# Optimization experiments

Measured on AMD Instinct MI355X. Metric: run time of the kernel, lower is better.

Reference implementation:

```python
import jax, jax.numpy as jnp
import numpy as np

EMB_DIM = 600
NN_UNITS = 300
K_FM = 5
B, L = 8, 2048


def fm(x, w0, w, V):
    # x: [B,L,F], w0: [1], w: [F], V: [k,F] -> [B,L,1]
    lin = w0 + x @ w[:, None]                      # [B,L,1]
    p1 = jnp.square(x @ V.T)                       # [B,L,k]
    p2 = jnp.square(x) @ jnp.square(V).T           # [B,L,k]
    inter = 0.5 * jnp.sum(p1 - p2, axis=-1, keepdims=True)
    return lin + inter


def setup_inputs() -> dict:
    key = jax.random.key(0)
    ks = jax.random.split(key, 12)
    s = 0.02
    inp = {
        "stack_input": jax.random.normal(ks[0], (2, B, L, EMB_DIM), jnp.float32),
        "W1": jax.random.normal(ks[1], (EMB_DIM, NN_UNITS), jnp.float32) * s,
        "b1": jnp.zeros((NN_UNITS,), jnp.float32),
        "W2": jax.random.normal(ks[2], (EMB_DIM, NN_UNITS), jnp.float32) * s,
        "b2": jnp.zeros((NN_UNITS,), jnp.float32),
        # FM params for the two concat branches (F = 2*EMB_DIM)
        "fm_cat_w0": jax.random.normal(ks[3], (2, 1), jnp.float32) * s,
        "fm_cat_w": jax.random.normal(ks[4], (2, 2 * EMB_DIM), jnp.float32) * s,
        "fm_cat_V": jax.random.normal(ks[5], (2, K_FM, 2 * EMB_DIM), jnp.float32) * s,
        # FM params for diff(passage,query) and mul(passage,query): order [p_diff, q_diff, p_mul, q_mul]
        "fm_dm_w0": jax.random.normal(ks[6], (4, 1), jnp.float32) * s,
        "fm_dm_w": jax.random.normal(ks[7], (4, EMB_DIM), jnp.float32) * s,
        "fm_dm_V": jax.random.normal(ks[8], (4, K_FM, EMB_DIM), jnp.float32) * s,
    }
    return inp


def reference(stack_input, W1, b1, W2, b2, fm_cat_w0, fm_cat_w, fm_cat_V,
              fm_dm_w0, fm_dm_w, fm_dm_V):
    passage = stack_input[0]   # [B,L,D]
    query = stack_input[1]     # [B,L,D]

    p_dense = jax.nn.relu(passage @ W1 + b1)   # [B,L,U]
    q_dense = jax.nn.relu(query @ W2 + b2)     # [B,L,U]

    scale = 1.0 / np.sqrt(EMB_DIM).astype(np.float32)
    affinity = scale * jnp.einsum('bpu,bqu->bpq', p_dense, q_dense)  # [B,Lp,Lq]

    aligned_p = jax.nn.softmax(affinity, axis=-1)                    # [B,Lp,Lq]
    aligned_q = jax.nn.softmax(jnp.swapaxes(affinity, 1, 2), axis=-1)  # [B,Lq,Lp]

    passage_aligned = jnp.einsum('bpq,bqd->bpd', aligned_p, passage)  # [B,Lp,D]
    query_aligned = jnp.einsum('bqp,bpd->bqd', aligned_q, query)      # [B,Lq,D]

    passage_concat = jnp.concatenate([query_aligned, passage], axis=2)
    query_concat = jnp.concatenate([passage_aligned, query], axis=2)
    passage_diff = query_aligned - passage
    query_diff = passage_aligned - query
    passage_mul = query_aligned * passage
    query_mul = passage_aligned * query

    c1 = fm(passage_concat, fm_cat_w0[0], fm_cat_w[0], fm_cat_V[0])
    c2 = fm(query_concat, fm_cat_w0[1], fm_cat_w[1], fm_cat_V[1])
    c3 = fm(passage_diff, fm_dm_w0[0], fm_dm_w[0], fm_dm_V[0])
    c4 = fm(query_diff, fm_dm_w0[1], fm_dm_w[1], fm_dm_V[1])
    c5 = fm(passage_mul, fm_dm_w0[2], fm_dm_w[2], fm_dm_V[2])
    c6 = fm(query_mul, fm_dm_w0[3], fm_dm_w[3], fm_dm_V[3])

    features_passage = jnp.concatenate([c1, c3, c5], axis=2)  # [B,L,3]
    features_query = jnp.concatenate([c2, c4, c6], axis=2)    # [B,L,3]
    return features_passage, features_query
```

## Files before the change

### kernel.cpp

```cpp
#include <hip/hip_runtime.h>
#include <hip/hip_bf16.h>

#define BATCH 8
#define LEN   2048
#define DIM   600
#define UNITS 300
#define BL    16384

typedef __attribute__((ext_vector_type(4))) float f32x4;
typedef __attribute__((ext_vector_type(8))) short s16x8;

#define PDB_OFF   0ULL
#define WT_OFF    20971520ULL
#define VT_OFF    21954560ULL
#define EXP_OFF   63897600ULL
#define EXPT_OFF  131006464ULL
#define PAB_OFF   198115328ULL
#define QAB_OFF   218038272ULL
#define RS_OFF    237961216ULL
#define CS_OFF    238026752ULL
#define WS_NEED   238092288ULL

#define AF_SCALE 0.040824829046386304f

__device__ __forceinline__ float wave_sum(float v) {
#pragma unroll
  for (int off = 32; off > 0; off >>= 1) v += __shfl_xor(v, off);
  return v;
}

__device__ __forceinline__ ushort f2bf(float f) {
  union { float f; uint u; } x; x.f = f;
  uint r = x.u + 0x7fffu + ((x.u >> 16) & 1u);
  return (ushort)(r >> 16);
}

__device__ __forceinline__ void ldbf8(const ushort* p, float* f) {
  uint4 q = *(const uint4*)p;
  f[0] = __uint_as_float(q.x << 16); f[1] = __uint_as_float(q.x & 0xffff0000u);
  f[2] = __uint_as_float(q.y << 16); f[3] = __uint_as_float(q.y & 0xffff0000u);
  f[4] = __uint_as_float(q.z << 16); f[5] = __uint_as_float(q.z & 0xffff0000u);
  f[6] = __uint_as_float(q.w << 16); f[7] = __uint_as_float(q.w & 0xffff0000u);
}
__device__ __forceinline__ void ldf8(const float* p, float* f) {
  float4 a = *(const float4*)p, b = *(const float4*)(p + 4);
  f[0]=a.x; f[1]=a.y; f[2]=a.z; f[3]=a.w; f[4]=b.x; f[5]=b.y; f[6]=b.z; f[7]=b.w;
}

__device__ __forceinline__ s16x8 pack8(float4 a, float4 b) {
  s16x8 r;
  r[0]=(short)f2bf(a.x); r[1]=(short)f2bf(a.y); r[2]=(short)f2bf(a.z); r[3]=(short)f2bf(a.w);
  r[4]=(short)f2bf(b.x); r[5]=(short)f2bf(b.y); r[6]=(short)f2bf(b.z); r[7]=(short)f2bf(b.w);
  return r;
}

__global__ __launch_bounds__(256) void prep_wt(const float* __restrict__ W1,
                                               const float* __restrict__ W2,
                                               char* __restrict__ wsb) {
  int id = blockIdx.x * 256 + threadIdx.x;
  if (id >= 2 * 384 * 80) return;
  int dir = id / (384 * 80); int rem = id % (384 * 80);
  int n = rem / 80, ko = rem % 80;
  const float* W = dir ? W2 : W1;
  s16x8 v;
#pragma unroll
  for (int e = 0; e < 8; e++) {
    int k = ko * 8 + e;
    float f = (n < 300 && k < 600) ? W[(size_t)k * 300 + n] : 0.f;
    v[e] = (short)f2bf(f);
  }
  ushort* wt = (ushort*)(wsb + WT_OFF) + (size_t)dir * 384 * 640 + (size_t)n * 640 + ko * 8;
  *(s16x8*)wt = v;
}

__global__ __launch_bounds__(256) void prep_vt(const float* __restrict__ stack,
                                               char* __restrict__ wsb) {
  int z = blockIdx.z;
  const float* src = stack + (size_t)z * LEN * DIM;
  ushort* dst = (ushort*)(wsb + VT_OFF) + (size_t)z * 640 * 2048;
  int p0 = blockIdx.x * 64, d0 = blockIdx.y * 64;
  __shared__ float tile[64][65];
  int t = threadIdx.x;
#pragma unroll
  for (int u = 0; u < 16; u++) {
    int id = u * 256 + t; int r = id >> 6, c = id & 63;
    tile[r][c] = (d0 + c < DIM) ? src[(size_t)(p0 + r) * DIM + d0 + c] : 0.f;
  }
  __syncthreads();
#pragma unroll
  for (int u = 0; u < 16; u++) {
    int id = u * 256 + t; int d = id >> 6, c = id & 63;
    dst[(size_t)(d0 + d) * 2048 + p0 + c] = f2bf(tile[c][d]);
  }
}

__global__ __launch_bounds__(256) void transp_bf16(char* __restrict__ wsb) {
  int b = blockIdx.z;
  const ushort* src = (const ushort*)(wsb + EXP_OFF) + (size_t)b * 2048 * 2048;
  ushort* dst = (ushort*)(wsb + EXPT_OFF) + (size_t)b * 2048 * 2048;
  int p0 = blockIdx.y * 64, q0 = blockIdx.x * 64;
  __shared__ ushort tile[64][72];
  int t = threadIdx.x;
#pragma unroll
  for (int u = 0; u < 2; u++) {
    int id = u * 256 + t; int r = id >> 3, c = id & 7;
    *(s16x8*)&tile[r][c * 8] = *(const s16x8*)(src + (size_t)(p0 + r) * 2048 + q0 + c * 8);
  }
  __syncthreads();
#pragma unroll
  for (int u = 0; u < 2; u++) {
    int id = u * 256 + t; int q = id >> 3, c = id & 7;
    s16x8 v;
#pragma unroll
    for (int e = 0; e < 8; e++) v[e] = (short)tile[c * 8 + e][q];
    *(s16x8*)(dst + (size_t)(q0 + q) * 2048 + p0 + c * 8) = v;
  }
}

template<int MODE>
__global__ __launch_bounds__(256) void gemm_nt(const float* __restrict__ stack,
                                               const float* __restrict__ b1,
                                               const float* __restrict__ b2,
                                               char* __restrict__ wsb) {
  constexpr int KS = (MODE == 0) ? 10 : ((MODE == 1) ? 5 : 32);
  const int t = threadIdx.x;
  const int g = (t >> 4) & 3, l16 = t & 15;
  const int wv = t >> 6, wr = wv >> 1, wc = wv & 1;
  __shared__ __align__(16) char smem[34816];
  char* Ab = smem;
  char* Bb = smem + 16384;

  const int z = blockIdx.z;
  const int m0 = blockIdx.y * 128, n0 = blockIdx.x * 128;

  const float* Agf = nullptr;
  const ushort* Agb = nullptr;
  const ushort* Bgb = nullptr;
  int lda = 0, ldb = 0;
  int dir = 0, bat = 0;
  if constexpr (MODE == 0) {
    Agf = stack + (size_t)z * BL * DIM; lda = DIM;
    Bgb = (const ushort*)(wsb + WT_OFF) + (size_t)z * 384 * 640; ldb = 640;
  } else if constexpr (MODE == 1) {
    Agb = (const ushort*)(wsb + PDB_OFF) + (size_t)z * 2048 * 320; lda = 320;
    Bgb = (const ushort*)(wsb + PDB_OFF) + (size_t)16384 * 320 + (size_t)z * 2048 * 320; ldb = 320;
  } else {
    dir = z & 1; bat = z >> 1;
    Agb = (const ushort*)(wsb + (dir ? EXPT_OFF : EXP_OFF)) + (size_t)bat * 2048 * 2048; lda = 2048;
    Bgb = (const ushort*)(wsb + VT_OFF) + ((size_t)dir * 8 + bat) * 640 * 2048; ldb = 2048;
  }

  f32x4 acc[4][4];
#pragma unroll
  for (int i = 0; i < 4; i++)
#pragma unroll
    for (int j = 0; j < 4; j++) { f32x4 zz = {0.f, 0.f, 0.f, 0.f}; acc[i][j] = zz; }

  for (int kt = 0; kt < KS; kt++) {
    int k0 = kt * 64;
#pragma unroll
    for (int u = 0; u < 4; u++) {
      int c = u * 256 + t; int row = c >> 3; int sl = c & 7; int gs = sl ^ (row & 7);
      s16x8 va;
      if constexpr (MODE == 0) {
        int kb = k0 + gs * 8;
        if (kb < DIM) {
          const float* s = Agf + (size_t)(m0 + row) * DIM + kb;
          va = pack8(*(const float4*)s, *(const float4*)(s + 4));
        } else {
          s16x8 zz = {0,0,0,0,0,0,0,0}; va = zz;
        }
      } else {
        va = *(const s16x8*)(Agb + (size_t)(m0 + row) * lda + k0 + gs * 8);
      }
      *(s16x8*)(Ab + row * 128 + sl * 16) = va;
      *(s16x8*)(Bb + row * 128 + sl * 16) =
          *(const s16x8*)(Bgb + (size_t)(n0 + row) * ldb + k0 + gs * 8);
    }
    __syncthreads();
#pragma unroll
    for (int ks = 0; ks < 2; ks++) {
      s16x8 af[4], bf[4];
#pragma unroll
      for (int f = 0; f < 4; f++) {
        int ar = wr * 64 + f * 16 + l16;
        af[f] = *(const s16x8*)(Ab + ar * 128 + (((ks * 4 + g) ^ (ar & 7)) * 16));
        int br = wc * 64 + f * 16 + l16;
        bf[f] = *(const s16x8*)(Bb + br * 128 + (((ks * 4 + g) ^ (br & 7)) * 16));
      }
#pragma unroll
      for (int i = 0; i < 4; i++)
#pragma unroll
        for (int j = 0; j < 4; j++)
          acc[i][j] = __builtin_amdgcn_mfma_f32_16x16x32_bf16(af[i], bf[j], acc[i][j], 0, 0, 0);
    }
    __syncthreads();
  }

  char* eb = smem;
  const float* bias = nullptr;
  const float* sums = nullptr;
  float* rowsum = nullptr; float* colsum = nullptr;
  if constexpr (MODE == 0) bias = z ? b2 : b1;
  if constexpr (MODE == 1) {
    rowsum = (float*)(wsb + RS_OFF) + (size_t)z * 2048;
    colsum = (float*)(wsb + CS_OFF) + (size_t)z * 2048;
  }
  if constexpr (MODE == 2)
    sums = (const float*)(wsb + (dir ? CS_OFF : RS_OFF)) + (size_t)bat * 2048;

  float colpart[4] = {0.f, 0.f, 0.f, 0.f};
#pragma unroll
  for (int fm = 0; fm < 4; fm++) {
#pragma unroll
    for (int i = 0; i < 4; i++) {
      int m = wr * 64 + fm * 16 + 4 * g + i;
      float inv = 1.f;
      if constexpr (MODE == 2) inv = 1.f / sums[m0 + m];
      float rowpart = 0.f;
#pragma unroll
      for (int fn = 0; fn < 4; fn++) {
        int n = wc * 64 + fn * 16 + l16;
        float v = acc[fm][fn][i];
        if constexpr (MODE == 0) {
          int gn = n0 + n;
          v = (gn < UNITS) ? fmaxf(v + bias[gn], 0.f) : 0.f;
        } else if constexpr (MODE == 1) {
          v = __expf(v * AF_SCALE);
          rowpart += v; colpart[fn] += v;
        } else {
          v *= inv;
        }
        *(ushort*)(eb + m * 272 + 2 * n) = f2bf(v);
      }
      if constexpr (MODE == 1) {
        rowpart += __shfl_xor(rowpart, 1);
        rowpart += __shfl_xor(rowpart, 2);
        rowpart += __shfl_xor(rowpart, 4);
        rowpart += __shfl_xor(rowpart, 8);
        if (l16 == 0) atomicAdd(&rowsum[m0 + m], rowpart);
      }
    }
  }
  if constexpr (MODE == 1) {
#pragma unroll
    for (int fn = 0; fn < 4; fn++) {
      float cp = colpart[fn];
      cp += __shfl_xor(cp, 16);
      cp += __shfl_xor(cp, 32);
      if (((t >> 4) & 3) == 0)
        atomicAdd(&colsum[n0 + wc * 64 + fn * 16 + l16], cp);
    }
  }
  __syncthreads();

#pragma unroll
  for (int u = 0; u < 8; u++) {
    int id = u * 256 + t; int m = id >> 4; int c = id & 15;
    s16x8 v = *(const s16x8*)(eb + m * 272 + c * 16);
    int gn = n0 + c * 8;
    if constexpr (MODE == 0) {
      if (gn < 320) {
        ushort* outp = (ushort*)(wsb + PDB_OFF) + (size_t)z * 16384 * 320;
        *(s16x8*)(outp + (size_t)(m0 + m) * 320 + gn) = v;
      }
    } else if constexpr (MODE == 1) {
      ushort* outp = (ushort*)(wsb + EXP_OFF) + (size_t)z * 2048 * 2048;
      *(s16x8*)(outp + (size_t)(m0 + m) * 2048 + gn) = v;
    } else {
      if (gn < 608) {
        ushort* outp = (ushort*)(wsb + (dir ? QAB_OFF : PAB_OFF)) + (size_t)bat * 2048 * 608;
        *(s16x8*)(outp + (size_t)(m0 + m) * 608 + gn) = v;
      }
    }
  }
}

__global__ __launch_bounds__(256) void fm_v2(
    const float* __restrict__ stack, const char* __restrict__ wsb,
    const float* __restrict__ cat_w0, const float* __restrict__ cat_w,
    const float* __restrict__ cat_V, const float* __restrict__ dm_w0,
    const float* __restrict__ dm_w, const float* __restrict__ dm_V,
    float* __restrict__ out)
{
  const int lane = threadIdx.x & 63;
  const int gw = blockIdx.x * 4 + (threadIdx.x >> 6);
  const int branch = gw >> 14;
  const int pos = gw & 16383;
  const ushort* x1 = (const ushort*)(wsb + (branch ? PAB_OFF : QAB_OFF)) + (size_t)pos * 608;
  const float* x2 = stack + (size_t)branch * BL * DIM + (size_t)pos * DIM;
  float* o = out + (size_t)branch * (BL * 3) + (size_t)pos * 3;

  {
    const float* w = cat_w + branch * 1200;
    const float* V = cat_V + (size_t)branch * 6000;
    float accW = 0.f, accP[5] = {}, accQ[5] = {};
    for (int oc = lane; oc < 150; oc += 64) {
      float x[8];
      if (oc < 75) ldbf8(x1 + oc * 8, x);
      else         ldf8(x2 + (oc - 75) * 8, x);
      float wv[8]; ldf8(w + oc * 8, wv);
#pragma unroll
      for (int e = 0; e < 8; e++) accW = fmaf(x[e], wv[e], accW);
#pragma unroll
      for (int k = 0; k < 5; k++) {
        float vv[8]; ldf8(V + k * 1200 + oc * 8, vv);
#pragma unroll
        for (int e = 0; e < 8; e++) {
          float xv = x[e] * vv[e];
          accP[k] += xv;
          accQ[k] = fmaf(xv, xv, accQ[k]);
        }
      }
    }
    float r = wave_sum(accW); float inter = 0.f;
#pragma unroll
    for (int k = 0; k < 5; k++) {
      float P = wave_sum(accP[k]), Q = wave_sum(accQ[k]);
      inter += P * P - Q;
    }
    if (lane == 0) o[0] = cat_w0[branch] + r + 0.5f * inter;
  }
#pragma unroll
  for (int which = 0; which < 2; which++) {
    const int idx = which * 2 + branch;
    const float* w = dm_w + idx * 600;
    const float* V = dm_V + (size_t)idx * 3000;
    float accW = 0.f, accP[5] = {}, accQ[5] = {};
    for (int oc = lane; oc < 75; oc += 64) {
      float a[8], b[8], x[8];
      ldbf8(x1 + oc * 8, a);
      ldf8(x2 + oc * 8, b);
#pragma unroll
      for (int e = 0; e < 8; e++) x[e] = which ? a[e] * b[e] : a[e] - b[e];
      float wv[8]; ldf8(w + oc * 8, wv);
#pragma unroll
      for (int e = 0; e < 8; e++) accW = fmaf(x[e], wv[e], accW);
#pragma unroll
      for (int k = 0; k < 5; k++) {
        float vv[8]; ldf8(V + k * 600 + oc * 8, vv);
#pragma unroll
        for (int e = 0; e < 8; e++) {
          float xv = x[e] * vv[e];
          accP[k] += xv;
          accQ[k] = fmaf(xv, xv, accQ[k]);
        }
      }
    }
    float r = wave_sum(accW); float inter = 0.f;
#pragma unroll
    for (int k = 0; k < 5; k++) {
      float P = wave_sum(accP[k]), Q = wave_sum(accQ[k]);
      inter += P * P - Q;
    }
    if (lane == 0) o[1 + which] = dm_w0[idx] + r + 0.5f * inter;
  }
}

#define PD_OFF   0UL
#define QD_OFF   4915200UL
#define PA_OFF   9830400UL
#define QA_OFF   19660800UL
#define A_OFF    29491200UL
#define ROWM_OFF 33685504UL
#define ROWS_OFF 33687552UL
#define COLM_OFF 33689600UL
#define COLS_OFF 33691648UL
#define PCM_OFF  33693696UL
#define PCS_OFF  33726464UL
#define WS_FB    (33759232UL * 4UL)

__global__ __launch_bounds__(256) void dense_kernel(
    const float* __restrict__ stack, const float* __restrict__ W1,
    const float* __restrict__ b1, const float* __restrict__ W2,
    const float* __restrict__ b2, float* __restrict__ ws)
{
  const int dir = blockIdx.z;
  const float* X = stack + (size_t)dir * BL * DIM;
  const float* W = dir ? W2 : W1;
  const float* bias = dir ? b2 : b1;
  float* C = ws + (dir ? QD_OFF : PD_OFF);
  const int m0 = blockIdx.y * 64;
  const int n0 = blockIdx.x * 64;
  __shared__ float As[32][68];
  __shared__ float Bs[32][68];
  const int t = threadIdx.x;
  const int tx = t & 15, ty = t >> 4;
  float acc[4][4] = {};
  for (int k0 = 0; k0 < DIM; k0 += 32) {
#pragma unroll
    for (int i = 0; i < 8; i++) {
      int idx = i * 256 + t;
      int m = idx >> 5, k = idx & 31;
      int kk = k0 + k;
      As[k][m] = (kk < DIM) ? X[(size_t)(m0 + m) * DIM + kk] : 0.f;
    }
#pragma unroll
    for (int i = 0; i < 8; i++) {
      int idx = i * 256 + t;
      int k = idx >> 6, n = idx & 63;
      int kk = k0 + k, nn = n0 + n;
      Bs[k][n] = (kk < DIM && nn < UNITS) ? W[(size_t)kk * UNITS + nn] : 0.f;
    }
    __syncthreads();
#pragma unroll
    for (int k = 0; k < 32; k++) {
      float a[4], bb[4];
#pragma unroll
      for (int i = 0; i < 4; i++) a[i] = As[k][ty * 4 + i];
#pragma unroll
      for (int j = 0; j < 4; j++) bb[j] = Bs[k][tx * 4 + j];
#pragma unroll
      for (int i = 0; i < 4; i++)
#pragma unroll
        for (int j = 0; j < 4; j++)
          acc[i][j] = fmaf(a[i], bb[j], acc[i][j]);
    }
    __syncthreads();
  }
#pragma unroll
  for (int j = 0; j < 4; j++) {
    int nn = n0 + tx * 4 + j;
    if (nn >= UNITS) continue;
    float bv = bias[nn];
#pragma unroll
    for (int i = 0; i < 4; i++) {
      int mm = m0 + ty * 4 + i;
      float v = acc[i][j] + bv;
      C[(size_t)mm * UNITS + nn] = v > 0.f ? v : 0.f;
    }
  }
}

__global__ __launch_bounds__(256) void affinity_kernel(float* __restrict__ ws, int b)
{
  const float* P = ws + PD_OFF + (size_t)b * LEN * UNITS;
  const float* Q = ws + QD_OFF + (size_t)b * LEN * UNITS;
  float* A = ws + A_OFF;
  const int p0 = blockIdx.y * 64;
  const int q0 = blockIdx.x * 64;
  __shared__ float As[32][68], Bs[32][68];
  const int t = threadIdx.x, tx = t & 15, ty = t >> 4;
  float acc[4][4] = {};
  for (int k0 = 0; k0 < UNITS; k0 += 32) {
#pragma unroll
    for (int i = 0; i < 8; i++) {
      int idx = i * 256 + t;
      int m = idx >> 5, k = idx & 31;
      int kk = k0 + k;
      As[k][m] = (kk < UNITS) ? P[(size_t)(p0 + m) * UNITS + kk] : 0.f;
      Bs[k][m] = (kk < UNITS) ? Q[(size_t)(q0 + m) * UNITS + kk] : 0.f;
    }
    __syncthreads();
#pragma unroll
    for (int k = 0; k < 32; k++) {
      float a[4], bb[4];
#pragma unroll
      for (int i = 0; i < 4; i++) a[i] = As[k][ty * 4 + i];
#pragma unroll
      for (int j = 0; j < 4; j++) bb[j] = Bs[k][tx * 4 + j];
#pragma unroll
      for (int i = 0; i < 4; i++)
#pragma unroll
        for (int j = 0; j < 4; j++)
          acc[i][j] = fmaf(a[i], bb[j], acc[i][j]);
    }
    __syncthreads();
  }
#pragma unroll
  for (int i = 0; i < 4; i++)
#pragma unroll
    for (int j = 0; j < 4; j++)
      A[(size_t)(p0 + ty * 4 + i) * LEN + (q0 + tx * 4 + j)] = acc[i][j] * AF_SCALE;
}

__global__ __launch_bounds__(256) void rowstats_kernel(float* __restrict__ ws)
{
  const float* A = ws + A_OFF;
  float* rowM = ws + ROWM_OFF;
  float* rowS = ws + ROWS_OFF;
  const int p = blockIdx.x;
  const int t = threadIdx.x;
  __shared__ float row[2048];
  __shared__ float red[256];
#pragma unroll
  for (int i = 0; i < 8; i++) row[i * 256 + t] = A[(size_t)p * LEN + i * 256 + t];
  __syncthreads();
  float pm = -3.0e38f;
#pragma unroll
  for (int i = 0; i < 8; i++) pm = fmaxf(pm, row[i * 256 + t]);
  red[t] = pm; __syncthreads();
  for (int off = 128; off > 0; off >>= 1) {
    if (t < off) red[t] = fmaxf(red[t], red[t + off]);
    __syncthreads();
  }
  float m = red[0];
  __syncthreads();
  float ps = 0.f;
#pragma unroll
  for (int i = 0; i < 8; i++) ps += __expf(row[i * 256 + t] - m);
  red[t] = ps; __syncthreads();
  for (int off = 128; off > 0; off >>= 1) {
    if (t < off) red[t] += red[t + off];
    __syncthreads();
  }
  if (t == 0) { rowM[p] = m; rowS[p] = 1.f / red[0]; }
}

__global__ __launch_bounds__(256) void colpart_kernel(float* __restrict__ ws)
{
  const float* A = ws + A_OFF;
  float* pcm = ws + PCM_OFF;
  float* pcs = ws + PCS_OFF;
  const int q = blockIdx.x * 256 + threadIdx.x;
  const int chunk = blockIdx.y;
  const int p0 = chunk * 128;
  float m = -3.0e38f, s = 0.f;
  for (int p = p0; p < p0 + 128; p++) {
    float v = A[(size_t)p * LEN + q];
    float nm = fmaxf(m, v);
    s = s * __expf(m - nm) + __expf(v - nm);
    m = nm;
  }
  pcm[chunk * 2048 + q] = m;
  pcs[chunk * 2048 + q] = s;
}

__global__ __launch_bounds__(256) void colcomb_kernel(float* __restrict__ ws)
{
  const float* pcm = ws + PCM_OFF;
  const float* pcs = ws + PCS_OFF;
  float* colM = ws + COLM_OFF;
  float* colS = ws + COLS_OFF;
  const int q = blockIdx.x * 256 + threadIdx.x;
  float m = -3.0e38f;
#pragma unroll
  for (int c = 0; c < 16; c++) m = fmaxf(m, pcm[c * 2048 + q]);
  float s = 0.f;
#pragma unroll
  for (int c = 0; c < 16; c++) s += pcs[c * 2048 + q] * __expf(pcm[c * 2048 + q] - m);
  colM[q] = m;
  colS[q] = 1.f / s;
}

__global__ __launch_bounds__(256) void aligned_kernel(const float* __restrict__ stack,
                                                      float* __restrict__ ws, int b)
{
  const int transA = blockIdx.z;
  const float* A = ws + A_OFF;
  const float* stM = ws + (transA ? COLM_OFF : ROWM_OFF);
  const float* stS = ws + (transA ? COLS_OFF : ROWS_OFF);
  const float* V = stack + (size_t)transA * BL * DIM + (size_t)b * LEN * DIM;
  float* O = ws + (transA ? QA_OFF : PA_OFF) + (size_t)b * LEN * DIM;
  const int m0 = blockIdx.y * 64;
  const int n0 = blockIdx.x * 64;
  __shared__ float As[32][68], Bs[32][68];
  __shared__ float sM[64], sS[64];
  const int t = threadIdx.x, tx = t & 15, ty = t >> 4;
  if (t < 64) { sM[t] = stM[m0 + t]; sS[t] = stS[m0 + t]; }
  __syncthreads();
  float acc[4][4] = {};
  for (int k0 = 0; k0 < LEN; k0 += 32) {
    if (!transA) {
#pragma unroll
      for (int i = 0; i < 8; i++) {
        int idx = i * 256 + t;
        int m = idx >> 5, k = idx & 31;
        float a = A[(size_t)(m0 + m) * LEN + k0 + k];
        As[k][m] = __expf(a - sM[m]) * sS[m];
      }
    } else {
#pragma unroll
      for (int i = 0; i < 8; i++) {
        int idx = i * 256 + t;
        int k = idx >> 6, m = idx & 63;
        float a = A[(size_t)(k0 + k) * LEN + m0 + m];
        As[k][m] = __expf(a - sM[m]) * sS[m];
      }
    }
#pragma unroll
    for (int i = 0; i < 8; i++) {
      int idx = i * 256 + t;
      int k = idx >> 6, n = idx & 63;
      int nn = n0 + n;
      Bs[k][n] = (nn < DIM) ? V[(size_t)(k0 + k) * DIM + nn] : 0.f;
    }
    __syncthreads();
#pragma unroll
    for (int k = 0; k < 32; k++) {
      float a[4], bb[4];
#pragma unroll
      for (int i = 0; i < 4; i++) a[i] = As[k][ty * 4 + i];
#pragma unroll
      for (int j = 0; j < 4; j++) bb[j] = Bs[k][tx * 4 + j];
#pragma unroll
      for (int i = 0; i < 4; i++)
#pragma unroll
        for (int j = 0; j < 4; j++)
          acc[i][j] = fmaf(a[i], bb[j], acc[i][j]);
    }
    __syncthreads();
  }
#pragma unroll
  for (int i = 0; i < 4; i++)
#pragma unroll
    for (int j = 0; j < 4; j++) {
      int nn = n0 + tx * 4 + j;
      if (nn < DIM) O[(size_t)(m0 + ty * 4 + i) * DIM + nn] = acc[i][j];
    }
}

__global__ __launch_bounds__(256) void fm_kernel(
    const float* __restrict__ stack, const float* __restrict__ ws,
    const float* __restrict__ cat_w0, const float* __restrict__ cat_w,
    const float* __restrict__ cat_V, const float* __restrict__ dm_w0,
    const float* __restrict__ dm_w, const float* __restrict__ dm_V,
    float* __restrict__ out)
{
  const int lane = threadIdx.x & 63;
  const int gw = blockIdx.x * 4 + (threadIdx.x >> 6);
  const int branch = gw >> 14;
  const int pos = gw & 16383;
  const float* x1 = ws + (branch ? PA_OFF : QA_OFF) + (size_t)pos * DIM;
  const float* x2 = stack + (size_t)branch * BL * DIM + (size_t)pos * DIM;
  float* o = out + (size_t)branch * (BL * 3) + (size_t)pos * 3;
  {
    const float* w = cat_w + branch * 1200;
    const float* Vm = cat_V + branch * 6000;
    float accW = 0.f, accP[5] = {}, accQ[5] = {};
    for (int j = lane; j < 1200; j += 64) {
      float x = (j < 600) ? x1[j] : x2[j - 600];
      accW = fmaf(x, w[j], accW);
      float xx = x * x;
#pragma unroll
      for (int k = 0; k < 5; k++) {
        float v = Vm[k * 1200 + j];
        accP[k] = fmaf(x, v, accP[k]);
        accQ[k] = fmaf(xx, v * v, accQ[k]);
      }
    }
    accW = wave_sum(accW);
    float inter = 0.f;
#pragma unroll
    for (int k = 0; k < 5; k++) {
      float P = wave_sum(accP[k]);
      float Qv = wave_sum(accQ[k]);
      inter += P * P - Qv;
    }
    if (lane == 0) o[0] = cat_w0[branch] + accW + 0.5f * inter;
  }
  {
    const float* w = dm_w + branch * 600;
    const float* Vm = dm_V + branch * 3000;
    float accW = 0.f, accP[5] = {}, accQ[5] = {};
    for (int j = lane; j < 600; j += 64) {
      float x = x1[j] - x2[j];
      accW = fmaf(x, w[j], accW);
      float xx = x * x;
#pragma unroll
      for (int k = 0; k < 5; k++) {
        float v = Vm[k * 600 + j];
        accP[k] = fmaf(x, v, accP[k]);
        accQ[k] = fmaf(xx, v * v, accQ[k]);
      }
    }
    accW = wave_sum(accW);
    float inter = 0.f;
#pragma unroll
    for (int k = 0; k < 5; k++) {
      float P = wave_sum(accP[k]);
      float Qv = wave_sum(accQ[k]);
      inter += P * P - Qv;
    }
    if (lane == 0) o[1] = dm_w0[branch] + accW + 0.5f * inter;
  }
  {
    const int idx4 = 2 + branch;
    const float* w = dm_w + idx4 * 600;
    const float* Vm = dm_V + idx4 * 3000;
    float accW = 0.f, accP[5] = {}, accQ[5] = {};
    for (int j = lane; j < 600; j += 64) {
      float x = x1[j] * x2[j];
      accW = fmaf(x, w[j], accW);
      float xx = x * x;
#pragma unroll
      for (int k = 0; k < 5; k++) {
        float v = Vm[k * 600 + j];
        accP[k] = fmaf(x, v, accP[k]);
        accQ[k] = fmaf(xx, v * v, accQ[k]);
      }
    }
    accW = wave_sum(accW);
    float inter = 0.f;
#pragma unroll
    for (int k = 0; k < 5; k++) {
      float P = wave_sum(accP[k]);
      float Qv = wave_sum(accQ[k]);
      inter += P * P - Qv;
    }
    if (lane == 0) o[2] = dm_w0[idx4] + accW + 0.5f * inter;
  }
}

extern "C" void kernel_launch(void* const* d_in, const int* in_sizes, int n_in,
                              void* d_out, int out_size, void* d_ws, size_t ws_size,
                              hipStream_t stream) {
  const float* stack  = (const float*)d_in[0];
  const float* W1     = (const float*)d_in[1];
  const float* b1     = (const float*)d_in[2];
  const float* W2     = (const float*)d_in[3];
  const float* b2     = (const float*)d_in[4];
  const float* cat_w0 = (const float*)d_in[5];
  const float* cat_w  = (const float*)d_in[6];
  const float* cat_V  = (const float*)d_in[7];
  const float* dm_w0  = (const float*)d_in[8];
  const float* dm_w   = (const float*)d_in[9];
  const float* dm_V   = (const float*)d_in[10];
  float* out = (float*)d_out;

  if (ws_size >= WS_NEED) {
    char* wsb = (char*)d_ws;
    hipMemsetAsync(wsb + RS_OFF, 0, 131072, stream);
    prep_wt<<<240, 256, 0, stream>>>(W1, W2, wsb);
    prep_vt<<<dim3(32, 10, 16), 256, 0, stream>>>(stack, wsb);
    gemm_nt<0><<<dim3(3, 128, 2), 256, 0, stream>>>(stack, b1, b2, wsb);
    gemm_nt<1><<<dim3(16, 16, 8), 256, 0, stream>>>(stack, b1, b2, wsb);
    transp_bf16<<<dim3(32, 32, 8), 256, 0, stream>>>(wsb);
    gemm_nt<2><<<dim3(5, 16, 16), 256, 0, stream>>>(stack, b1, b2, wsb);
    fm_v2<<<8192, 256, 0, stream>>>(stack, wsb, cat_w0, cat_w, cat_V,
                                    dm_w0, dm_w, dm_V, out);
  } else {
    float* ws = (float*)d_ws;
    dense_kernel<<<dim3(5, 256, 2), 256, 0, stream>>>(stack, W1, b1, W2, b2, ws);
    for (int b = 0; b < BATCH; b++) {
      affinity_kernel<<<dim3(32, 32), 256, 0, stream>>>(ws, b);
      rowstats_kernel<<<2048, 256, 0, stream>>>(ws);
      colpart_kernel<<<dim3(8, 16), 256, 0, stream>>>(ws);
      colcomb_kernel<<<8, 256, 0, stream>>>(ws);
      aligned_kernel<<<dim3(10, 32, 2), 256, 0, stream>>>(stack, ws, b);
    }
    fm_kernel<<<8192, 256, 0, stream>>>(stack, ws, cat_w0, cat_w, cat_V,
                                        dm_w0, dm_w, dm_V, out);
  }
}
```

Before: 597.1 us.

## Fuse transpose into affinity GEMM epilogue, prefetch tiles, remap blocks per XCD

The separate bf16 transpose kernel is removed. The affinity GEMM epilogue now also writes the transposed exp tile straight from LDS, using a swizzled LDS layout to avoid bank conflicts on the column reads. The GEMM main loop now prefetches the next K tile into registers while the MFMAs run on the current tile. Blocks are launched as a 1D grid and remapped so that consecutive tiles land on the same XCD. Together these aim to cut a full round trip through global memory, hide load latency, and improve L2 locality, at the cost of more registers and a larger epilogue.

```diff
diff --git a/kernel.cpp b/kernel.cpp
--- a/kernel.cpp
+++ b/kernel.cpp
@@ -54,6 +54,10 @@
   return r;
 }
 
+__device__ __forceinline__ int eboff(int m, int n) {
+  return m * 272 + ((((n >> 3) ^ ((m >> 3) & 7)) << 4) | ((n & 7) << 1));
+}
+
 __global__ __launch_bounds__(256) void prep_wt(const float* __restrict__ W1,
                                                const float* __restrict__ W2,
                                                char* __restrict__ wsb) {
@@ -91,29 +95,6 @@
   for (int u = 0; u < 16; u++) {
     int id = u * 256 + t; int d = id >> 6, c = id & 63;
     dst[(size_t)(d0 + d) * 2048 + p0 + c] = f2bf(tile[c][d]);
-  }
-}
-
-__global__ __launch_bounds__(256) void transp_bf16(char* __restrict__ wsb) {
-  int b = blockIdx.z;
-  const ushort* src = (const ushort*)(wsb + EXP_OFF) + (size_t)b * 2048 * 2048;
-  ushort* dst = (ushort*)(wsb + EXPT_OFF) + (size_t)b * 2048 * 2048;
-  int p0 = blockIdx.y * 64, q0 = blockIdx.x * 64;
-  __shared__ ushort tile[64][72];
-  int t = threadIdx.x;
-#pragma unroll
-  for (int u = 0; u < 2; u++) {
-    int id = u * 256 + t; int r = id >> 3, c = id & 7;
-    *(s16x8*)&tile[r][c * 8] = *(const s16x8*)(src + (size_t)(p0 + r) * 2048 + q0 + c * 8);
-  }
-  __syncthreads();
-#pragma unroll
-  for (int u = 0; u < 2; u++) {
-    int id = u * 256 + t; int q = id >> 3, c = id & 7;
-    s16x8 v;
-#pragma unroll
-    for (int e = 0; e < 8; e++) v[e] = (short)tile[c * 8 + e][q];
-    *(s16x8*)(dst + (size_t)(q0 + q) * 2048 + p0 + c * 8) = v;
   }
 }
 
@@ -130,8 +111,22 @@
   char* Ab = smem;
   char* Bb = smem + 16384;
 
-  const int z = blockIdx.z;
-  const int m0 = blockIdx.y * 128, n0 = blockIdx.x * 128;
+  int bx, by, bz;
+  {
+    int bid = blockIdx.x;
+    if constexpr (MODE == 0) {
+      int s = (bid & 7) * 96 + (bid >> 3);
+      bx = s % 3; by = (s / 3) & 127; bz = s / 384;
+    } else if constexpr (MODE == 1) {
+      int s = (bid & 7) * 256 + (bid >> 3);
+      bx = s & 15; by = (s >> 4) & 15; bz = s >> 8;
+    } else {
+      int s = (bid & 7) * 160 + (bid >> 3);
+      bx = s % 5; by = (s / 5) & 15; bz = s / 80;
+    }
+  }
+  const int z = bz;
+  const int m0 = by * 128, n0 = bx * 128;
 
   const float* Agf = nullptr;
   const ushort* Agb = nullptr;
@@ -150,34 +145,44 @@
     Bgb = (const ushort*)(wsb + VT_OFF) + ((size_t)dir * 8 + bat) * 640 * 2048; ldb = 2048;
   }
 
-  f32x4 acc[4][4];
-#pragma unroll
-  for (int i = 0; i < 4; i++)
-#pragma unroll
-    for (int j = 0; j < 4; j++) { f32x4 zz = {0.f, 0.f, 0.f, 0.f}; acc[i][j] = zz; }
-
-  for (int kt = 0; kt < KS; kt++) {
-    int k0 = kt * 64;
+  auto load_regs = [&](int k0, s16x8* va, s16x8* vb) {
 #pragma unroll
     for (int u = 0; u < 4; u++) {
       int c = u * 256 + t; int row = c >> 3; int sl = c & 7; int gs = sl ^ (row & 7);
-      s16x8 va;
       if constexpr (MODE == 0) {
         int kb = k0 + gs * 8;
         if (kb < DIM) {
           const float* s = Agf + (size_t)(m0 + row) * DIM + kb;
-          va = pack8(*(const float4*)s, *(const float4*)(s + 4));
+          va[u] = pack8(*(const float4*)s, *(const float4*)(s + 4));
         } else {
-          s16x8 zz = {0,0,0,0,0,0,0,0}; va = zz;
+          s16x8 zz = {0,0,0,0,0,0,0,0}; va[u] = zz;
         }
       } else {
-        va = *(const s16x8*)(Agb + (size_t)(m0 + row) * lda + k0 + gs * 8);
-      }
-      *(s16x8*)(Ab + row * 128 + sl * 16) = va;
-      *(s16x8*)(Bb + row * 128 + sl * 16) =
-          *(const s16x8*)(Bgb + (size_t)(n0 + row) * ldb + k0 + gs * 8);
-    }
-    __syncthreads();
+        va[u] = *(const s16x8*)(Agb + (size_t)(m0 + row) * lda + k0 + gs * 8);
+      }
+      vb[u] = *(const s16x8*)(Bgb + (size_t)(n0 + row) * ldb + k0 + gs * 8);
+    }
+  };
+
+  f32x4 acc[4][4];
+#pragma unroll
+  for (int i = 0; i < 4; i++)
+#pragma unroll
+    for (int j = 0; j < 4; j++) { f32x4 zz = {0.f, 0.f, 0.f, 0.f}; acc[i][j] = zz; }
+
+  s16x8 va[4], vb[4];
+  load_regs(0, va, vb);
+
+  for (int kt = 0; kt < KS; kt++) {
+#pragma unroll
+    for (int u = 0; u < 4; u++) {
+      int c = u * 256 + t; int row = c >> 3; int sl = c & 7;
+      *(s16x8*)(Ab + row * 128 + sl * 16) = va[u];
+      *(s16x8*)(Bb + row * 128 + sl * 16) = vb[u];
+    }
+    __syncthreads();
+    s16x8 na[4], nb[4];
+    if (kt + 1 < KS) load_regs((kt + 1) * 64, na, nb);
 #pragma unroll
     for (int ks = 0; ks < 2; ks++) {
       s16x8 af[4], bf[4];
@@ -195,6 +200,8 @@
           acc[i][j] = __builtin_amdgcn_mfma_f32_16x16x32_bf16(af[i], bf[j], acc[i][j], 0, 0, 0);
     }
     __syncthreads();
+#pragma unroll
+    for (int u = 0; u < 4; u++) { va[u] = na[u]; vb[u] = nb[u]; }
   }
 
   char* eb = smem;
@@ -231,7 +238,7 @@
         } else {
           v *= inv;
         }
-        *(ushort*)(eb + m * 272 + 2 * n) = f2bf(v);
+        *(ushort*)(eb + eboff(m, n)) = f2bf(v);
       }
       if constexpr (MODE == 1) {
         rowpart += __shfl_xor(rowpart, 1);
@@ -256,9 +263,9 @@
 
 #pragma unroll
   for (int u = 0; u < 8; u++) {
-    int id = u * 256 + t; int m = id >> 4; int c = id & 15;
-    s16x8 v = *(const s16x8*)(eb + m * 272 + c * 16);
-    int gn = n0 + c * 8;
+    int id = u * 256 + t; int m = id >> 4; int cn = id & 15;
+    s16x8 v = *(const s16x8*)(eb + m * 272 + ((cn ^ ((m >> 3) & 7)) << 4));
+    int gn = n0 + cn * 8;
     if constexpr (MODE == 0) {
       if (gn < 320) {
         ushort* outp = (ushort*)(wsb + PDB_OFF) + (size_t)z * 16384 * 320;
@@ -272,6 +279,19 @@
         ushort* outp = (ushort*)(wsb + (dir ? QAB_OFF : PAB_OFF)) + (size_t)bat * 2048 * 608;
         *(s16x8*)(outp + (size_t)(m0 + m) * 608 + gn) = v;
       }
+    }
+  }
+
+  if constexpr (MODE == 1) {
+    ushort* outpT = (ushort*)(wsb + EXPT_OFF) + (size_t)z * 2048 * 2048;
+#pragma unroll
+    for (int u = 0; u < 8; u++) {
+      int id = u * 256 + t; int n = id >> 4; int mb = (id & 15) * 8;
+      s16x8 v;
+#pragma unroll
+      for (int e = 0; e < 8; e++)
+        v[e] = *(const short*)(eb + eboff(mb + e, n));
+      *(s16x8*)(outpT + (size_t)(n0 + n) * 2048 + m0 + mb) = v;
     }
   }
 }
@@ -368,7 +388,6 @@
 #define COLS_OFF 33691648UL
 #define PCM_OFF  33693696UL
 #define PCS_OFF  33726464UL
-#define WS_FB    (33759232UL * 4UL)
 
 __global__ __launch_bounds__(256) void dense_kernel(
     const float* __restrict__ stack, const float* __restrict__ W1,
@@ -723,10 +742,9 @@
     hipMemsetAsync(wsb + RS_OFF, 0, 131072, stream);
     prep_wt<<<240, 256, 0, stream>>>(W1, W2, wsb);
     prep_vt<<<dim3(32, 10, 16), 256, 0, stream>>>(stack, wsb);
-    gemm_nt<0><<<dim3(3, 128, 2), 256, 0, stream>>>(stack, b1, b2, wsb);
-    gemm_nt<1><<<dim3(16, 16, 8), 256, 0, stream>>>(stack, b1, b2, wsb);
-    transp_bf16<<<dim3(32, 32, 8), 256, 0, stream>>>(wsb);
-    gemm_nt<2><<<dim3(5, 16, 16), 256, 0, stream>>>(stack, b1, b2, wsb);
+    gemm_nt<0><<<768, 256, 0, stream>>>(stack, b1, b2, wsb);
+    gemm_nt<1><<<2048, 256, 0, stream>>>(stack, b1, b2, wsb);
+    gemm_nt<2><<<1280, 256, 0, stream>>>(stack, b1, b2, wsb);
     fm_v2<<<8192, 256, 0, stream>>>(stack, wsb, cat_w0, cat_w, cat_V,
                                     dm_w0, dm_w, dm_V, out);
   } else {
```

After: 556.9 us. 6.7% less time.
